# Optimization experiments

Hardware: AMD Instinct MI355X
Metric: run time of the kernel (lower is better)

Reference implementation:

```python
import jax, jax.numpy as jnp
import numpy as np
import math

D_MODEL = 512
D_STATE = 64  # N; state uses N//2 complex modes
BATCH = 8
SEQ = 4096
DT_MIN, DT_MAX = 1e-3, 1e-1


def setup_inputs() -> dict:
    key = jax.random.key(0)
    ks = jax.random.split(key, 8)
    H, N2 = D_MODEL, D_STATE // 2
    x = jax.random.normal(ks[0], (BATCH, SEQ, D_MODEL), dtype=jnp.float32)
    log_dt = jax.random.uniform(ks[1], (H,), dtype=jnp.float32) * (math.log(DT_MAX) - math.log(DT_MIN)) + math.log(DT_MIN)
    # A = -0.5 + i*pi*n  ->  A_real_log = log(0.5)
    A_real_log = jnp.full((H, N2), math.log(0.5), dtype=jnp.float32)
    A_imag = jnp.tile(jnp.arange(N2, dtype=jnp.float32) * math.pi, (H, 1))
    B_re = jax.random.normal(ks[2], (H, N2), dtype=jnp.float32)
    B_im = jax.random.normal(ks[3], (H, N2), dtype=jnp.float32)
    C_re = jax.random.normal(ks[4], (H, N2), dtype=jnp.float32)
    C_im = jax.random.normal(ks[5], (H, N2), dtype=jnp.float32)
    D = jax.random.normal(ks[6], (H,), dtype=jnp.float32)
    return {"x": x, "log_dt": log_dt, "A_real_log": A_real_log, "A_imag": A_imag,
            "B_re": B_re, "B_im": B_im, "C_re": C_re, "C_im": C_im, "D": D}


def _s4d_scan(x, log_dt, A_real_log, A_imag, B_re, B_im, C_re, C_im, D):
    # ZOH discretization (setup_step)
    dt = jnp.exp(log_dt)                                 # (H,)
    A = -jnp.exp(A_real_log) + 1j * A_imag               # (H, N2) complex
    dtA = A * dt[:, None]
    dA = jnp.exp(dtA)                                    # (H, N2)
    Bc = B_re + 1j * B_im
    Cc = C_re + 1j * C_im
    dB = Bc * (jnp.expm1(dtA) / A)                       # (H, N2)

    Bsz = x.shape[0]
    state0 = jnp.zeros((Bsz, x.shape[2], dA.shape[1]), dtype=jnp.complex64)

    def step(state, x_t):  # x_t: (B, H)
        state = dA * state + dB * x_t[..., None]         # (B, H, N2)
        y = 2.0 * jnp.real(jnp.einsum('hn,bhn->bh', Cc, state)) + D * x_t
        return state, jax.nn.gelu(y, approximate=False)

    final_state, ys = jax.lax.scan(step, state0, jnp.swapaxes(x, 0, 1))  # ys: (L, B, H)
    return jnp.swapaxes(ys, 0, 1), final_state


def reference(x, log_dt, A_real_log, A_imag, B_re, B_im, C_re, C_im, D):
    return _s4d_scan(x, log_dt, A_real_log, A_imag, B_re, B_im, C_re, C_im, D)
```

## Files before the change

### kernel.cpp

```cpp
#include <hip/hip_runtime.h>
#include <math.h>


#define H_  512
#define L_  4096
#define B_  8
#define N2_ 32
#define NC  64
#define RSTR 72

typedef _Float16 f16;
typedef _Float16 f16x8 __attribute__((ext_vector_type(8)));
typedef _Float16 f16x4 __attribute__((ext_vector_type(4)));
typedef _Float16 f16x2 __attribute__((ext_vector_type(2)));
typedef float    f32x4 __attribute__((ext_vector_type(4)));

__device__ __forceinline__ float bfly1(float v) {
    return __int_as_float(__builtin_amdgcn_update_dpp(
        0, __float_as_int(v), 0xB1, 0xf, 0xf, true));
}

__global__ __launch_bounds__(256) void k_build(
    const float* __restrict__ log_dt,
    const float* __restrict__ A_real_log,
    const float* __restrict__ A_imag,
    const float* __restrict__ B_re,
    const float* __restrict__ B_im,
    const float* __restrict__ C_re,
    const float* __restrict__ C_im,
    const float* __restrict__ Dv,
    f16*  __restrict__ G,
    float* __restrict__ Lg)
{
    __shared__ float pr[32 * 66], pi[32 * 66];
    __shared__ float s_xr[32], s_xi[32], s_dBr[32], s_dBi[32],
                     s_wr[32], s_wi[32], s_wdr[32], s_wdi[32], s_k[64];
    const int h   = (int)blockIdx.x;
    const int tid = threadIdx.x;

    if (tid < 32) {
        const int n = tid, hn = h * N2_ + n;
        const float dt = expf(log_dt[h]);
        const float Ar = -expf(A_real_log[hn]);
        const float Ai = A_imag[hn];
        const float xr = dt * Ar, xi = dt * Ai;
        s_xr[n] = xr; s_xi[n] = xi;
        const float ex = expf(xr), cs = cosf(xi), sn = sinf(xi);
        const float sh  = sinf(0.5f * xi);
        const float emr = expm1f(xr) * cs - 2.0f * sh * sh;
        const float emi = ex * sn;
        const float ia  = 1.0f / (Ar * Ar + Ai * Ai);
        const float tr  = (emr * Ar + emi * Ai) * ia;
        const float ti  = (emi * Ar - emr * Ai) * ia;
        const float Brv = B_re[hn], Biv = B_im[hn];
        const float dBr = Brv * tr - Biv * ti, dBi = Brv * ti + Biv * tr;
        s_dBr[n] = dBr; s_dBi[n] = dBi;
        const float wr = 2.0f * C_re[hn], wi = 2.0f * C_im[hn];
        s_wr[n] = wr; s_wi[n] = wi;
        s_wdr[n] = wr * dBr - wi * dBi;
        s_wdi[n] = wr * dBi + wi * dBr;
    }
    __syncthreads();

    for (int e = tid; e < 2048; e += 256) {
        const int n = e >> 6, p = e & 63;
        const float ex = expf((float)p * s_xr[n]);
        float sn, cs; sincosf((float)p * s_xi[n], &sn, &cs);
        pr[n * 66 + p] = ex * cs; pi[n * 66 + p] = ex * sn;
    }
    if (tid < 32) {
        const int n = tid;
        const float ex = expf(64.f * s_xr[n]);
        float sn, cs; sincosf(64.f * s_xi[n], &sn, &cs);
        pr[n * 66 + 64] = ex * cs; pi[n * 66 + 64] = ex * sn;
    }
    __syncthreads();

    if (tid < 64) {
        float acc = 0.f;
        for (int n = 0; n < 32; ++n)
            acc += s_wdr[n] * pr[n * 66 + tid] - s_wdi[n] * pi[n * 66 + tid];
        s_k[tid] = acc;
    }
    if (tid < 32) {
        Lg[h * 64 + tid]      = pr[tid * 66 + 64];
        Lg[h * 64 + 32 + tid] = pi[tid * 66 + 64];
    }
    const float Dh = Dv[h];
    f16* Gh = G + (size_t)h * 192 * 64;
    for (int e = tid; e < 4096; e += 256) {
        const int t = e >> 6, j = e & 63, n = j >> 1;
        const float re = pr[n * 66 + t + 1], im = pi[n * 66 + t + 1];
        const float mv = (j & 1) ? -(s_wr[n] * im + s_wi[n] * re)
                                 :  (s_wr[n] * re - s_wi[n] * im);
        Gh[(size_t)(64 + t) * 64 + j] = (f16)mv;
    }
    for (int e = tid; e < 4096; e += 256) {
        const int r = e >> 6, s = e & 63, n = r >> 1;
        const float re = pr[n * 66 + 63 - s], im = pi[n * 66 + 63 - s];
        const float vv = (r & 1) ? (s_dBr[n] * im + s_dBi[n] * re)
                                 : (s_dBr[n] * re - s_dBi[n] * im);
        Gh[(size_t)(128 + r) * 64 + s] = (f16)vv;
    }
    __syncthreads();
    for (int e = tid; e < 4096; e += 256) {
        const int t = e >> 6, s = e & 63;
        const float tv = (s <= t) ? (s_k[t - s] + (s == t ? Dh : 0.f)) : 0.f;
        Gh[(size_t)t * 64 + s] = (f16)tv;
    }
}

__global__ __launch_bounds__(512, 4) void s4d_conv_kernel(
    const float* __restrict__ x,
    const f16*  __restrict__ G,
    const float* __restrict__ Lg,
    float* __restrict__ y,
    float* __restrict__ st_re,
    float* __restrict__ st_im)
{
    __shared__ f16 XT[8][64][RSTR];

    const int bid = (int)blockIdx.x;
    const int lb  = (bid & 7) * 64 + (bid >> 3);
    const int hg  = lb >> 3;
    const int b   = lb & 7;

    const int tid = threadIdx.x;
    const int l   = tid & 63;
    const int w   = tid >> 6;
    const int h   = hg * 8 + w;
    const int row16 = l & 15, kg = l >> 4;

    const f16* Gh = G + (size_t)h * 192 * 64;

    f16x8 Vf[4][2];
#pragma unroll
    for (int mt = 0; mt < 4; ++mt)
#pragma unroll
        for (int ks = 0; ks < 2; ++ks)
            Vf[mt][ks] = *(const f16x8*)
                &Gh[(size_t)(128 + mt * 16 + row16) * 64 + ks * 32 + kg * 8];
    const float lr  = Lg[h * 64 + (l >> 1)];
    const float li0 = Lg[h * 64 + 32 + (l >> 1)];
    const float lis = (l & 1) ? li0 : -li0;

    const int h_off = (tid & 1) * 4;
    const int tp    = tid >> 1;
    const float* xb_ = x + (size_t)b * L_ * H_ + hg * 8;
#pragma unroll 2
    for (int iter = 0; iter < 8; ++iter) {
        const int t0 = iter * 512 + tp * 2;
        const f32x4 v0 = *(const f32x4*)&xb_[(size_t)t0 * H_ + h_off];
        const f32x4 v1 = *(const f32x4*)&xb_[(size_t)(t0 + 1) * H_ + h_off];
        const int c = t0 >> 6, s0 = t0 & 63;
#pragma unroll
        for (int j = 0; j < 4; ++j) {
            f16x2 p; p[0] = (f16)v0[j]; p[1] = (f16)v1[j];
            *(f16x2*)&XT[h_off + j][c][s0] = p;
        }
    }
    __syncthreads();

    f16 (*Xw)[RSTR] = XT[w];

    f16x8 xbA[4], xbB[4];
#pragma unroll
    for (int nt = 0; nt < 4; ++nt) {
        const int col = nt * 16 + row16;
        xbA[nt] = *(const f16x8*)&Xw[col][kg * 8];
        xbB[nt] = *(const f16x8*)&Xw[col][32 + kg * 8];
        f32x4 ac0 = {0.f,0.f,0.f,0.f}, ac1 = {0.f,0.f,0.f,0.f},
              ac2 = {0.f,0.f,0.f,0.f}, ac3 = {0.f,0.f,0.f,0.f};
        ac0 = __builtin_amdgcn_mfma_f32_16x16x32_f16(Vf[0][0], xbA[nt], ac0, 0,0,0);
        ac0 = __builtin_amdgcn_mfma_f32_16x16x32_f16(Vf[0][1], xbB[nt], ac0, 0,0,0);
        ac1 = __builtin_amdgcn_mfma_f32_16x16x32_f16(Vf[1][0], xbA[nt], ac1, 0,0,0);
        ac1 = __builtin_amdgcn_mfma_f32_16x16x32_f16(Vf[1][1], xbB[nt], ac1, 0,0,0);
        ac2 = __builtin_amdgcn_mfma_f32_16x16x32_f16(Vf[2][0], xbA[nt], ac2, 0,0,0);
        ac2 = __builtin_amdgcn_mfma_f32_16x16x32_f16(Vf[2][1], xbB[nt], ac2, 0,0,0);
        ac3 = __builtin_amdgcn_mfma_f32_16x16x32_f16(Vf[3][0], xbA[nt], ac3, 0,0,0);
        ac3 = __builtin_amdgcn_mfma_f32_16x16x32_f16(Vf[3][1], xbB[nt], ac3, 0,0,0);
        const f32x4 a4[4] = {ac0, ac1, ac2, ac3};
#pragma unroll
        for (int mt = 0; mt < 4; ++mt) {
            f16x4 pv;
            pv[0] = (f16)a4[mt][0]; pv[1] = (f16)a4[mt][1];
            pv[2] = (f16)a4[mt][2]; pv[3] = (f16)a4[mt][3];
            *(f16x4*)&Xw[col][mt * 16 + kg * 4] = pv;
        }
    }

    {
        const int j = l, n = j >> 1;
        float u = 0.f;
        for (int c0 = 0; c0 < NC; c0 += 8) {
            float pv[8];
#pragma unroll
            for (int k2 = 0; k2 < 8; ++k2)
                pv[k2] = (float)Xw[c0 + k2][j];
#pragma unroll
            for (int k2 = 0; k2 < 8; ++k2) {
                Xw[c0 + k2][j] = (f16)u;
                const float usw = bfly1(u);
                u = fmaf(lr, u, fmaf(lis, usw, pv[k2]));
            }
        }
        const int pairIdx = b * H_ + h;
        if ((j & 1) == 0) st_re[(size_t)pairIdx * N2_ + n] = u;
        else              st_im[(size_t)pairIdx * N2_ + n] = u;
    }

    {
        f16x8 ub0[4], ub1[4];
#pragma unroll
        for (int nt = 0; nt < 4; ++nt) {
            const int col = nt * 16 + row16;
            ub0[nt] = *(const f16x8*)&Xw[col][kg * 8];
            ub1[nt] = *(const f16x8*)&Xw[col][32 + kg * 8];
        }
#pragma unroll
        for (int mt = 0; mt < 4; ++mt) {
            const size_t rT = (size_t)(mt * 16 + row16) * 64;
            const size_t rM = (size_t)(64 + mt * 16 + row16) * 64;
            const f16x8 Tf0 = *(const f16x8*)&Gh[rT + kg * 8];
            const f16x8 Tf1 = *(const f16x8*)&Gh[rT + 32 + kg * 8];
            const f16x8 Mf0 = *(const f16x8*)&Gh[rM + kg * 8];
            const f16x8 Mf1 = *(const f16x8*)&Gh[rM + 32 + kg * 8];
#pragma unroll
            for (int nt = 0; nt < 4; ++nt) {
                const int col = nt * 16 + row16;
                f32x4 ac = {0.f, 0.f, 0.f, 0.f};
                ac = __builtin_amdgcn_mfma_f32_16x16x32_f16(Tf0, xbA[nt], ac, 0,0,0);
                ac = __builtin_amdgcn_mfma_f32_16x16x32_f16(Tf1, xbB[nt], ac, 0,0,0);
                ac = __builtin_amdgcn_mfma_f32_16x16x32_f16(Mf0, ub0[nt], ac, 0,0,0);
                ac = __builtin_amdgcn_mfma_f32_16x16x32_f16(Mf1, ub1[nt], ac, 0,0,0);
                const int t0 = mt * 16 + kg * 4;
                f16x4 pk;
#pragma unroll
                for (int r = 0; r < 4; ++r) {
                    const float yv = ac[r];
                    const float y2 = yv * yv;
                    const float arg = yv * fmaf(-0.10294502f, y2, -2.30218425f);
                    const float e   = __builtin_amdgcn_exp2f(arg);
                    pk[r] = (f16)(yv * __builtin_amdgcn_rcpf(1.0f + e));
                }
                *(f16x4*)&Xw[col][t0] = pk;
            }
        }
    }
    __syncthreads();

    {
        float* yb_ = y + (size_t)b * L_ * H_ + hg * 8;
#pragma unroll 2
        for (int iter = 0; iter < 8; ++iter) {
            const int t0 = iter * 512 + tp * 2;
            const int c = t0 >> 6, s0 = t0 & 63;
            f32x4 v0, v1;
#pragma unroll
            for (int j = 0; j < 4; ++j) {
                const f16x2 p = *(const f16x2*)&XT[h_off + j][c][s0];
                v0[j] = (float)p[0]; v1[j] = (float)p[1];
            }
            *(f32x4*)&yb_[(size_t)t0 * H_ + h_off]       = v0;
            *(f32x4*)&yb_[(size_t)(t0 + 1) * H_ + h_off] = v1;
        }
    }
}

extern "C" void kernel_launch(void* const* d_in, const int* in_sizes, int n_in,
                              void* d_out, int out_size, void* d_ws, size_t ws_size,
                              hipStream_t stream) {
    (void)in_sizes; (void)n_in; (void)out_size; (void)ws_size;
    const float* x    = (const float*)d_in[0];
    const float* ldt  = (const float*)d_in[1];
    const float* Arl  = (const float*)d_in[2];
    const float* Aim  = (const float*)d_in[3];
    const float* Bre  = (const float*)d_in[4];
    const float* Bim  = (const float*)d_in[5];
    const float* Cre  = (const float*)d_in[6];
    const float* Cim  = (const float*)d_in[7];
    const float* Dv   = (const float*)d_in[8];
    float* out = (float*)d_out;
    float* st_re = out + (size_t)B_ * L_ * H_;
    float* st_im = st_re + (size_t)B_ * H_ * N2_;

    f16*   G  = (f16*)d_ws;
    float* Lg = (float*)((char*)d_ws + (size_t)H_ * 192 * 64 * 2);

    hipLaunchKernelGGL(k_build, dim3(H_), dim3(256), 0, stream,
                       ldt, Arl, Aim, Bre, Bim, Cre, Cim, Dv, G, Lg);
    hipLaunchKernelGGL(s4d_conv_kernel, dim3(512), dim3(512), 0, stream,
                       x, G, Lg, out, st_re, st_im);
}
```

Baseline: 162.3 us.

## Process 16 heads per block with 1024 threads for wider coalesced x/y rows

```diff
diff --git a/kernel.cpp b/kernel.cpp
--- a/kernel.cpp
+++ b/kernel.cpp
@@ -8,6 +8,7 @@
 #define N2_ 32
 #define NC  64
 #define RSTR 72
+#define TSTR 4624
 
 typedef _Float16 f16;
 typedef _Float16 f16x8 __attribute__((ext_vector_type(8)));
@@ -110,7 +111,7 @@
     }
 }
 
-__global__ __launch_bounds__(512, 4) void s4d_conv_kernel(
+__global__ __launch_bounds__(1024, 4) void s4d_conv_kernel(
     const float* __restrict__ x,
     const f16*  __restrict__ G,
     const float* __restrict__ Lg,
@@ -118,17 +119,17 @@
     float* __restrict__ st_re,
     float* __restrict__ st_im)
 {
-    __shared__ f16 XT[8][64][RSTR];
+    __shared__ f16 XT[16 * TSTR];
 
     const int bid = (int)blockIdx.x;
-    const int lb  = (bid & 7) * 64 + (bid >> 3);
+    const int lb  = (bid & 7) * 32 + (bid >> 3);
     const int hg  = lb >> 3;
     const int b   = lb & 7;
 
     const int tid = threadIdx.x;
     const int l   = tid & 63;
     const int w   = tid >> 6;
-    const int h   = hg * 8 + w;
+    const int h   = hg * 16 + w;
     const int row16 = l & 15, kg = l >> 4;
 
     const f16* Gh = G + (size_t)h * 192 * 64;
@@ -144,31 +145,31 @@
     const float li0 = Lg[h * 64 + 32 + (l >> 1)];
     const float lis = (l & 1) ? li0 : -li0;
 
-    const int h_off = (tid & 1) * 4;
-    const int tp    = tid >> 1;
-    const float* xb_ = x + (size_t)b * L_ * H_ + hg * 8;
+    const int hq = tid & 3;
+    const int tp = tid >> 2;
+    const float* xb_ = x + (size_t)b * L_ * H_ + hg * 16 + hq * 4;
 #pragma unroll 2
     for (int iter = 0; iter < 8; ++iter) {
         const int t0 = iter * 512 + tp * 2;
-        const f32x4 v0 = *(const f32x4*)&xb_[(size_t)t0 * H_ + h_off];
-        const f32x4 v1 = *(const f32x4*)&xb_[(size_t)(t0 + 1) * H_ + h_off];
+        const f32x4 v0 = *(const f32x4*)&xb_[(size_t)t0 * H_];
+        const f32x4 v1 = *(const f32x4*)&xb_[(size_t)(t0 + 1) * H_];
         const int c = t0 >> 6, s0 = t0 & 63;
 #pragma unroll
         for (int j = 0; j < 4; ++j) {
             f16x2 p; p[0] = (f16)v0[j]; p[1] = (f16)v1[j];
-            *(f16x2*)&XT[h_off + j][c][s0] = p;
-        }
-    }
-    __syncthreads();
-
-    f16 (*Xw)[RSTR] = XT[w];
+            *(f16x2*)&XT[((j << 2) | hq) * TSTR + c * RSTR + s0] = p;
+        }
+    }
+    __syncthreads();
+
+    f16* Xw = &XT[(((w & 3) << 2) | (w >> 2)) * TSTR];
 
     f16x8 xbA[4], xbB[4];
 #pragma unroll
     for (int nt = 0; nt < 4; ++nt) {
         const int col = nt * 16 + row16;
-        xbA[nt] = *(const f16x8*)&Xw[col][kg * 8];
-        xbB[nt] = *(const f16x8*)&Xw[col][32 + kg * 8];
+        xbA[nt] = *(const f16x8*)&Xw[col * RSTR + kg * 8];
+        xbB[nt] = *(const f16x8*)&Xw[col * RSTR + 32 + kg * 8];
         f32x4 ac0 = {0.f,0.f,0.f,0.f}, ac1 = {0.f,0.f,0.f,0.f},
               ac2 = {0.f,0.f,0.f,0.f}, ac3 = {0.f,0.f,0.f,0.f};
         ac0 = __builtin_amdgcn_mfma_f32_16x16x32_f16(Vf[0][0], xbA[nt], ac0, 0,0,0);
@@ -185,7 +186,7 @@
             f16x4 pv;
             pv[0] = (f16)a4[mt][0]; pv[1] = (f16)a4[mt][1];
             pv[2] = (f16)a4[mt][2]; pv[3] = (f16)a4[mt][3];
-            *(f16x4*)&Xw[col][mt * 16 + kg * 4] = pv;
+            *(f16x4*)&Xw[col * RSTR + mt * 16 + kg * 4] = pv;
         }
     }
 
@@ -196,10 +197,10 @@
             float pv[8];
 #pragma unroll
             for (int k2 = 0; k2 < 8; ++k2)
-                pv[k2] = (float)Xw[c0 + k2][j];
+                pv[k2] = (float)Xw[(c0 + k2) * RSTR + j];
 #pragma unroll
             for (int k2 = 0; k2 < 8; ++k2) {
-                Xw[c0 + k2][j] = (f16)u;
+                Xw[(c0 + k2) * RSTR + j] = (f16)u;
                 const float usw = bfly1(u);
                 u = fmaf(lr, u, fmaf(lis, usw, pv[k2]));
             }
@@ -214,8 +215,8 @@
 #pragma unroll
         for (int nt = 0; nt < 4; ++nt) {
             const int col = nt * 16 + row16;
-            ub0[nt] = *(const f16x8*)&Xw[col][kg * 8];
-            ub1[nt] = *(const f16x8*)&Xw[col][32 + kg * 8];
+            ub0[nt] = *(const f16x8*)&Xw[col * RSTR + kg * 8];
+            ub1[nt] = *(const f16x8*)&Xw[col * RSTR + 32 + kg * 8];
         }
 #pragma unroll
         for (int mt = 0; mt < 4; ++mt) {
@@ -243,14 +244,14 @@
                     const float e   = __builtin_amdgcn_exp2f(arg);
                     pk[r] = (f16)(yv * __builtin_amdgcn_rcpf(1.0f + e));
                 }
-                *(f16x4*)&Xw[col][t0] = pk;
+                *(f16x4*)&Xw[col * RSTR + t0] = pk;
             }
         }
     }
     __syncthreads();
 
     {
-        float* yb_ = y + (size_t)b * L_ * H_ + hg * 8;
+        float* yb_ = y + (size_t)b * L_ * H_ + hg * 16 + hq * 4;
 #pragma unroll 2
         for (int iter = 0; iter < 8; ++iter) {
             const int t0 = iter * 512 + tp * 2;
@@ -258,11 +259,12 @@
             f32x4 v0, v1;
 #pragma unroll
             for (int j = 0; j < 4; ++j) {
-                const f16x2 p = *(const f16x2*)&XT[h_off + j][c][s0];
+                const f16x2 p = *(const f16x2*)
+                    &XT[((j << 2) | hq) * TSTR + c * RSTR + s0];
                 v0[j] = (float)p[0]; v1[j] = (float)p[1];
             }
-            *(f32x4*)&yb_[(size_t)t0 * H_ + h_off]       = v0;
-            *(f32x4*)&yb_[(size_t)(t0 + 1) * H_ + h_off] = v1;
+            *(f32x4*)&yb_[(size_t)t0 * H_]       = v0;
+            *(f32x4*)&yb_[(size_t)(t0 + 1) * H_] = v1;
         }
     }
 }
@@ -289,6 +291,6 @@
 
     hipLaunchKernelGGL(k_build, dim3(H_), dim3(256), 0, stream,
                        ldt, Arl, Aim, Bre, Bim, Cre, Cim, Dv, G, Lg);
-    hipLaunchKernelGGL(s4d_conv_kernel, dim3(512), dim3(512), 0, stream,
+    hipLaunchKernelGGL(s4d_conv_kernel, dim3(256), dim3(1024), 0, stream,
                        x, G, Lg, out, st_re, st_im);
 }
```

Result: faster. 153.6 us (-5.4%).
